# Performance work log

Measured on AMD Instinct MI355X. Metric: run time of the kernel, lower is better.

The kernel has to match this reference:

```python
import jax, jax.numpy as jnp
import numpy as np

DECAY = 0.99
EPS = 1e-05
COMMIT_COST = 0.25


def setup_inputs() -> dict:
    key = jax.random.key(0)
    k1, k2 = jax.random.split(key)
    z = jax.random.normal(k1, (32, 256, 64, 64), dtype=jnp.float32)
    codebook = jax.random.normal(k2, (512, 256), dtype=jnp.float32)
    n_i = jnp.zeros((512,), dtype=jnp.float32)
    e_i = codebook  # register_buffer('e_i', codebook.data.clone())
    return {"z": z, "codebook": codebook, "n_i": n_i, "e_i": e_i}


def reference(z, codebook, n_i, e_i):
    K, D = codebook.shape
    b = z.shape[0]
    flat = z.reshape(-1, D)  # [N, D]

    dist = (
        jnp.sum(flat * flat, axis=1, keepdims=True)
        + jnp.sum(codebook * codebook, axis=1)
        - 2.0 * (flat @ codebook.T)
    )  # [N, K]
    encoding = jnp.argmin(dist, axis=1)  # [N]

    # one-hot matmul gather == direct gather
    code = codebook[encoding].reshape(z.shape)

    # EMA codebook update (training path, no-grad in the original)
    counts = jax.ops.segment_sum(
        jnp.ones((flat.shape[0],), dtype=flat.dtype), encoding, num_segments=K
    )  # idx.sum(0)
    code_update = jax.ops.segment_sum(flat, encoding, num_segments=K)  # idx.T @ flat
    n_new = DECAY * n_i + (1.0 - DECAY) * counts
    n_new = (n_new + EPS) / (b + K * EPS) * b  # Laplace smoothing (uses batch size b)
    e_new = DECAY * e_i + (1.0 - DECAY) * code_update
    codebook_new = e_new / n_new[:, None]

    commitment_loss = COMMIT_COST * jnp.mean(
        (z - jax.lax.stop_gradient(code)) ** 2
    )
    # straight-through estimator
    code_ste = z + jax.lax.stop_gradient(code - z)
    return (code_ste, commitment_loss, encoding, codebook_new, n_new, e_new)
```

## Files before the change

### kernel.cpp

```cpp
#include <hip/hip_runtime.h>
#include <cfloat>

#define NROWS 131072
#define DIM 256
#define KCODES 512
#define DECAYF 0.99f
#define OMDECAYF 0.01f
#define EPSF 1e-5f
#define BATCHF 32.0f

#define CHUNK 128
#define ROWMASK 0x1FFFF

#define BMW 16
#define NWAVE 8
#define BMB (NWAVE * BMW)
#define PLANE_STRIDE (KCODES * DIM)
#define PLANE_BYTES (PLANE_STRIDE * 2)
#define PC2 16
#define NPIECE (KCODES / PC2)
#define PIECE_H_BYTES 8192
#define SBUF_HALF 16384

typedef __attribute__((ext_vector_type(8))) _Float16 half8;
typedef __attribute__((ext_vector_type(4))) float f32x4;


__device__ __forceinline__ void gload_lds16(const void* g, void* l) {
  __builtin_amdgcn_global_load_lds(
      (const __attribute__((address_space(1))) unsigned int*)g,
      (__attribute__((address_space(3))) unsigned int*)l, 16, 0, 0);
}

__global__ __launch_bounds__(256) void cnorm_kernel(const float* __restrict__ cb,
                                                    const float* __restrict__ e_i,
                                                    float* __restrict__ cnorm,
                                                    float* __restrict__ en_out,
                                                    unsigned short* __restrict__ planes,
                                                    int* __restrict__ counts,
                                                    int* __restrict__ off,
                                                    float* __restrict__ loss_acc) {
  int k = blockIdx.x;
  int t = threadIdx.x;
  if (t == 0) {
    counts[k] = 0;
    off[k] = 0;
    if (k == 0) loss_acc[0] = 0.f;
  }
  size_t idx = (size_t)k * DIM + t;
  float v = cb[idx];
  en_out[idx] = DECAYF * e_i[idx];
  _Float16 h = (_Float16)v;
  float r1 = v - (float)h;
  _Float16 m = (_Float16)r1;
  unsigned short hb, mb;
  __builtin_memcpy(&hb, &h, 2);
  __builtin_memcpy(&mb, &m, 2);
  int tile = k >> 4, cl = k & 15;
  int kc = t >> 5, lk = (t >> 3) & 3, j = t & 7;
  size_t faddr = ((size_t)((tile * 8 + kc) * 64 + lk * 16 + cl)) * 8 + j;
  planes[faddr] = hb;
  planes[PLANE_STRIDE + faddr] = mb;
  float s = v * v;
  for (int o = 32; o > 0; o >>= 1) s += __shfl_down(s, o);
  __shared__ float p[4];
  if ((t & 63) == 0) p[t >> 6] = s;
  __syncthreads();
  if (t == 0) cnorm[k] = (p[0] + p[1]) + (p[2] + p[3]);
}

__global__ __launch_bounds__(512, 4) void argmin_kernel(
    const float* __restrict__ z, const unsigned short* __restrict__ planes,
    const float* __restrict__ cnorm, const float* __restrict__ cb,
    int* __restrict__ enc_int, float* __restrict__ enc_out,
    int* __restrict__ counts, float* __restrict__ code_out,
    float* __restrict__ loss_acc) {
  __shared__ __align__(16) unsigned char sbuf[2 * SBUF_HALF];
  __shared__ float cn_s[KCODES];
  __shared__ int hist[KCODES];
  __shared__ int sm_enc[BMB];
  __shared__ float lds_loss;

  const int tid = threadIdx.x;
  const int w = tid >> 6;
  const int l = tid & 63;
  const int lc = l & 15;
  const int lk = l >> 4;

  hist[tid] = 0;
  cn_s[tid] = cnorm[tid];
  if (tid == 0) lds_loss = 0.f;

  half8 a_h[8], a_m[8];
  float zn = 0.f;
  {
    int row = blockIdx.x * BMB + w * BMW + lc;
    const float* zr = z + (size_t)row * DIM;
#pragma unroll
    for (int ch = 0; ch < 8; ++ch) {
      float4 v0 = *(const float4*)&zr[ch * 32 + lk * 8];
      float4 v1 = *(const float4*)&zr[ch * 32 + lk * 8 + 4];
      float vv[8] = {v0.x, v0.y, v0.z, v0.w, v1.x, v1.y, v1.z, v1.w};
      half8 hh, mm;
#pragma unroll
      for (int j = 0; j < 8; ++j) {
        float f = vv[j];
        zn += f * f;
        _Float16 hb = (_Float16)f;
        float r1 = f - (float)hb;
        hh[j] = hb;
        mm[j] = (_Float16)r1;
      }
      a_h[ch] = hh; a_m[ch] = mm;
    }
  }
  zn += __shfl_xor(zn, 16);
  zn += __shfl_xor(zn, 32);

  float minv[4];
  int mini[4];
#pragma unroll
  for (int q = 0; q < 4; ++q) { minv[q] = FLT_MAX; mini[q] = 0; }

  const unsigned char* gplanes = (const unsigned char*)planes;

#define STAGE(p, b)                                                              \
  {                                                                              \
    const unsigned char* gh = gplanes + (size_t)(p) * PIECE_H_BYTES;             \
    unsigned char* lb = &sbuf[(b) * SBUF_HALF];                                  \
    _Pragma("unroll")                                                            \
    for (int q = 0; q < 2; ++q) {                                                \
      int c = w * 2 + q;                                                         \
      const unsigned char* g = (w < 4)                                           \
          ? gh + c * 1024 + l * 16                                               \
          : gh + PLANE_BYTES + (c - 8) * 1024 + l * 16;                          \
      gload_lds16(g, lb + c * 1024);                                             \
    }                                                                            \
  }

  STAGE(0, 0);
  __syncthreads();

#pragma unroll 1
  for (int p = 0; p < NPIECE; ++p) {
    const int cur = p & 1;
    if (p + 1 < NPIECE) STAGE(p + 1, cur ^ 1);

    const int lbase = cur * SBUF_HALF;
    f32x4 acc_a = {0.f, 0.f, 0.f, 0.f};
    f32x4 acc_b = {0.f, 0.f, 0.f, 0.f};
#pragma unroll
    for (int kc = 0; kc < 8; ++kc) {
      int o = lbase + kc * 1024 + l * 16;
      half8 bh = *(const half8*)&sbuf[o];
      half8 bm = *(const half8*)&sbuf[o + 8192];
      acc_a = __builtin_amdgcn_mfma_f32_16x16x32_f16(a_h[kc], bh, acc_a, 0, 0, 0);
      acc_b = __builtin_amdgcn_mfma_f32_16x16x32_f16(a_m[kc], bh, acc_b, 0, 0, 0);
      acc_a = __builtin_amdgcn_mfma_f32_16x16x32_f16(a_h[kc], bm, acc_a, 0, 0, 0);
    }
    {
      int code = p * PC2 + lc;
      float cn = cn_s[code];
#pragma unroll
      for (int q = 0; q < 4; ++q) {
        float s0 = cn - 2.f * (acc_a[q] + acc_b[q]);
        if (s0 < minv[q]) { minv[q] = s0; mini[q] = code; }
      }
    }
    __syncthreads();
  }
#undef STAGE


  float lsum = 0.f;
#pragma unroll
  for (int q = 0; q < 4; ++q) {
    float v = minv[q];
    int idx = mini[q];
    for (int o = 1; o < 16; o <<= 1) {
      float ov = __shfl_xor(v, o);
      int oi = __shfl_xor(idx, o);
      if (ov < v || (ov == v && oi < idx)) { v = ov; idx = oi; }
    }
    float znq = __shfl(zn, lk * 4 + q);
    if (lc == 0) {
      int rloc = w * BMW + lk * 4 + q;
      int row = blockIdx.x * BMB + rloc;
      enc_int[row] = idx;
      enc_out[row] = (float)idx;
      sm_enc[rloc] = idx;
      atomicAdd(&hist[idx], 1);
      lsum += znq + v;
    }
  }
  {
    float val = (lc == 0) ? lsum : 0.f;
    val += __shfl_xor(val, 16);
    val += __shfl_xor(val, 32);
    if (l == 0) atomicAdd(&lds_loss, val);
  }
  __syncthreads();

  {
    const float4* cb4 = (const float4*)cb;
    float4* out4 = (float4*)code_out;
    int base = blockIdx.x * (BMB * (DIM / 4));
#pragma unroll
    for (int it = 0; it < 16; ++it) {
      int idx = it * 512 + tid;
      int k = sm_enc[idx >> 6];
      out4[base + idx] = cb4[k * (DIM / 4) + (idx & 63)];
    }
  }

  {
    int h0 = hist[tid];
    if (h0) atomicAdd(&counts[tid], h0);
  }
  if (tid == 0) atomicAdd(loss_acc, lds_loss);
}

__global__ __launch_bounds__(256) void scatter_kernel(
    const int* __restrict__ enc, const int* __restrict__ counts,
    int* __restrict__ off, int* __restrict__ rowlist) {
  __shared__ int lcnt[KCODES];
  __shared__ int lbase[KCODES];
  __shared__ int pref[KCODES];
  int tid = threadIdx.x;
  int row = blockIdx.x * 256 + tid;
  lcnt[tid] = 0;
  lcnt[tid + 256] = 0;
  pref[tid] = counts[tid];
  pref[tid + 256] = counts[tid + 256];
  __syncthreads();
  int k = enc[row];
  int p = atomicAdd(&lcnt[k], 1);
  for (int o = 1; o < KCODES; o <<= 1) {
    int v0 = (tid >= o) ? pref[tid - o] : 0;
    int v1 = (tid + 256 >= o) ? pref[tid + 256 - o] : 0;
    __syncthreads();
    pref[tid] += v0;
    pref[tid + 256] += v1;
    __syncthreads();
  }
  int c0 = lcnt[tid];
  if (c0) lbase[tid] = (pref[tid] - counts[tid]) + atomicAdd(&off[tid], c0);
  int c1 = lcnt[tid + 256];
  if (c1) lbase[tid + 256] = (pref[tid + 256] - counts[tid + 256]) + atomicAdd(&off[tid + 256], c1);
  __syncthreads();
  rowlist[lbase[k] + p] = (k << 17) | row;
}

__global__ __launch_bounds__(256) void chunk_sum_kernel(
    const float* __restrict__ z, const int* __restrict__ rowlist,
    float* __restrict__ en_out) {
  __shared__ int rl[CHUNK];
  int tid = threadIdx.x;
  int d = tid;
  if (tid < CHUNK) rl[tid] = rowlist[blockIdx.x * CHUNK + tid];
  __syncthreads();
  int cur = rl[0] >> 17;
  float s = 0.f;
  for (int i = 0; i < CHUNK; i += 4) {
    int p0 = rl[i + 0], p1 = rl[i + 1], p2 = rl[i + 2], p3 = rl[i + 3];
    float v0 = z[(size_t)(p0 & ROWMASK) * DIM + d];
    float v1 = z[(size_t)(p1 & ROWMASK) * DIM + d];
    float v2 = z[(size_t)(p2 & ROWMASK) * DIM + d];
    float v3 = z[(size_t)(p3 & ROWMASK) * DIM + d];
    int k;
    k = p0 >> 17;
    if (k != cur) { atomicAdd(&en_out[(size_t)cur * DIM + d], OMDECAYF * s); s = 0.f; cur = k; }
    s += v0;
    k = p1 >> 17;
    if (k != cur) { atomicAdd(&en_out[(size_t)cur * DIM + d], OMDECAYF * s); s = 0.f; cur = k; }
    s += v1;
    k = p2 >> 17;
    if (k != cur) { atomicAdd(&en_out[(size_t)cur * DIM + d], OMDECAYF * s); s = 0.f; cur = k; }
    s += v2;
    k = p3 >> 17;
    if (k != cur) { atomicAdd(&en_out[(size_t)cur * DIM + d], OMDECAYF * s); s = 0.f; cur = k; }
    s += v3;
  }
  atomicAdd(&en_out[(size_t)cur * DIM + d], OMDECAYF * s);
}

__global__ __launch_bounds__(256) void finalize_kernel(
    const float* __restrict__ en, const int* __restrict__ counts,
    const float* __restrict__ n_i, float* __restrict__ nn_out,
    float* __restrict__ cbn_out, const float* __restrict__ loss_acc,
    float* __restrict__ loss_out) {
  int k = blockIdx.x;
  int d = threadIdx.x;
  float nn = DECAYF * n_i[k] + OMDECAYF * (float)counts[k];
  nn = (nn + EPSF) / (BATCHF + (float)KCODES * EPSF) * BATCHF;
  if (d == 0) nn_out[k] = nn;
  size_t idx = (size_t)k * DIM + d;
  cbn_out[idx] = en[idx] / nn;
  if (k == 0 && d == 0) loss_out[0] = 0.25f * loss_acc[0] / 33554432.0f;
}

extern "C" void kernel_launch(void* const* d_in, const int* in_sizes, int n_in,
                              void* d_out, int out_size, void* d_ws, size_t ws_size,
                              hipStream_t stream) {
  const float* z = (const float*)d_in[0];
  const float* cb = (const float*)d_in[1];
  const float* n_i = (const float*)d_in[2];
  const float* e_i = (const float*)d_in[3];

  float* out = (float*)d_out;
  float* out_code = out;
  float* out_loss = out + 33554432;
  float* out_enc = out + 33554433;
  float* out_cbn = out + 33685505;
  float* out_nn = out + 33816577;
  float* out_en = out + 33817089;

  char* ws = (char*)d_ws;
  float* cnorm = (float*)(ws + 0);
  int* counts = (int*)(ws + 2048);
  float* loss_acc = (float*)(ws + 4096);
  int* off = (int*)(ws + 6144);
  int* enc_int = (int*)(ws + 12288);
  int* rowlist = (int*)(ws + 536576);
  unsigned short* planes = (unsigned short*)(ws + 536576);

  cnorm_kernel<<<KCODES, 256, 0, stream>>>(cb, e_i, cnorm, out_en, planes,
                                           counts, off, loss_acc);
  argmin_kernel<<<NROWS / BMB, 512, 0, stream>>>(z, planes, cnorm, cb, enc_int,
                                                 out_enc, counts, out_code, loss_acc);
  scatter_kernel<<<NROWS / 256, 256, 0, stream>>>(enc_int, counts, off, rowlist);
  chunk_sum_kernel<<<NROWS / CHUNK, 256, 0, stream>>>(z, rowlist, out_en);
  finalize_kernel<<<KCODES, 256, 0, stream>>>(out_en, counts, n_i, out_nn,
                                              out_cbn, loss_acc, out_loss);
}
```

Before: 362.5 us.

## Triple-buffer codebook pieces with explicit vmcnt waits and MFMA priority

```diff
diff --git a/kernel.cpp b/kernel.cpp
--- a/kernel.cpp
+++ b/kernel.cpp
@@ -21,6 +21,7 @@
 #define NPIECE (KCODES / PC2)
 #define PIECE_H_BYTES 8192
 #define SBUF_HALF 16384
+#define NBUF 3
 
 typedef __attribute__((ext_vector_type(8))) _Float16 half8;
 typedef __attribute__((ext_vector_type(4))) float f32x4;
@@ -75,11 +76,9 @@
     int* __restrict__ enc_int, float* __restrict__ enc_out,
     int* __restrict__ counts, float* __restrict__ code_out,
     float* __restrict__ loss_acc) {
-  __shared__ __align__(16) unsigned char sbuf[2 * SBUF_HALF];
+  __shared__ __align__(16) unsigned char sbuf[NBUF * SBUF_HALF];
   __shared__ float cn_s[KCODES];
-  __shared__ int hist[KCODES];
   __shared__ int sm_enc[BMB];
-  __shared__ float lds_loss;
 
   const int tid = threadIdx.x;
   const int w = tid >> 6;
@@ -87,9 +86,7 @@
   const int lc = l & 15;
   const int lk = l >> 4;
 
-  hist[tid] = 0;
   cn_s[tid] = cnorm[tid];
-  if (tid == 0) lds_loss = 0.f;
 
   half8 a_h[8], a_m[8];
   float zn = 0.f;
@@ -138,38 +135,51 @@
     }                                                                            \
   }
 
+#define COMPUTE(p)                                                               \
+  {                                                                              \
+    const int lbase = ((p) % NBUF) * SBUF_HALF;                                  \
+    f32x4 acc_a = {0.f, 0.f, 0.f, 0.f};                                          \
+    f32x4 acc_b = {0.f, 0.f, 0.f, 0.f};                                          \
+    __builtin_amdgcn_s_setprio(1);                                               \
+    _Pragma("unroll")                                                            \
+    for (int kc = 0; kc < 8; ++kc) {                                             \
+      int o = lbase + kc * 1024 + l * 16;                                        \
+      half8 bh = *(const half8*)&sbuf[o];                                        \
+      half8 bm = *(const half8*)&sbuf[o + 8192];                                 \
+      acc_a = __builtin_amdgcn_mfma_f32_16x16x32_f16(a_h[kc], bh, acc_a, 0, 0, 0); \
+      acc_b = __builtin_amdgcn_mfma_f32_16x16x32_f16(a_m[kc], bh, acc_b, 0, 0, 0); \
+      acc_a = __builtin_amdgcn_mfma_f32_16x16x32_f16(a_h[kc], bm, acc_a, 0, 0, 0); \
+    }                                                                            \
+    __builtin_amdgcn_s_setprio(0);                                               \
+    int code = (p) * PC2 + lc;                                                   \
+    float cn = cn_s[code];                                                       \
+    _Pragma("unroll")                                                            \
+    for (int q = 0; q < 4; ++q) {                                                \
+      float s0 = cn - 2.f * (acc_a[q] + acc_b[q]);                               \
+      if (s0 < minv[q]) { minv[q] = s0; mini[q] = code; }                        \
+    }                                                                            \
+  }
+
   STAGE(0, 0);
+  STAGE(1, 1);
   __syncthreads();
 
 #pragma unroll 1
-  for (int p = 0; p < NPIECE; ++p) {
-    const int cur = p & 1;
-    if (p + 1 < NPIECE) STAGE(p + 1, cur ^ 1);
-
-    const int lbase = cur * SBUF_HALF;
-    f32x4 acc_a = {0.f, 0.f, 0.f, 0.f};
-    f32x4 acc_b = {0.f, 0.f, 0.f, 0.f};
-#pragma unroll
-    for (int kc = 0; kc < 8; ++kc) {
-      int o = lbase + kc * 1024 + l * 16;
-      half8 bh = *(const half8*)&sbuf[o];
-      half8 bm = *(const half8*)&sbuf[o + 8192];
-      acc_a = __builtin_amdgcn_mfma_f32_16x16x32_f16(a_h[kc], bh, acc_a, 0, 0, 0);
-      acc_b = __builtin_amdgcn_mfma_f32_16x16x32_f16(a_m[kc], bh, acc_b, 0, 0, 0);
-      acc_a = __builtin_amdgcn_mfma_f32_16x16x32_f16(a_h[kc], bm, acc_a, 0, 0, 0);
-    }
-    {
-      int code = p * PC2 + lc;
-      float cn = cn_s[code];
-#pragma unroll
-      for (int q = 0; q < 4; ++q) {
-        float s0 = cn - 2.f * (acc_a[q] + acc_b[q]);
-        if (s0 < minv[q]) { minv[q] = s0; mini[q] = code; }
-      }
-    }
-    __syncthreads();
-  }
+  for (int p = 0; p < NPIECE - 1; ++p) {
+    if (p) {
+      asm volatile("s_waitcnt vmcnt(2)" ::: "memory");
+      __builtin_amdgcn_s_barrier();
+      __builtin_amdgcn_sched_barrier(0);
+    }
+    if (p + 2 < NPIECE) STAGE(p + 2, (p + 2) % NBUF);
+    COMPUTE(p);
+  }
+  asm volatile("s_waitcnt vmcnt(0)" ::: "memory");
+  __builtin_amdgcn_s_barrier();
+  __builtin_amdgcn_sched_barrier(0);
+  COMPUTE(NPIECE - 1);
 #undef STAGE
+#undef COMPUTE
 
 
   float lsum = 0.f;
@@ -189,7 +199,7 @@
       enc_int[row] = idx;
       enc_out[row] = (float)idx;
       sm_enc[rloc] = idx;
-      atomicAdd(&hist[idx], 1);
+      atomicAdd(&counts[idx], 1);
       lsum += znq + v;
     }
   }
@@ -197,7 +207,7 @@
     float val = (lc == 0) ? lsum : 0.f;
     val += __shfl_xor(val, 16);
     val += __shfl_xor(val, 32);
-    if (l == 0) atomicAdd(&lds_loss, val);
+    if (l == 0) atomicAdd(loss_acc, val);
   }
   __syncthreads();
 
@@ -212,12 +222,6 @@
       out4[base + idx] = cb4[k * (DIM / 4) + (idx & 63)];
     }
   }
-
-  {
-    int h0 = hist[tid];
-    if (h0) atomicAdd(&counts[tid], h0);
-  }
-  if (tid == 0) atomicAdd(loss_acc, lds_loss);
 }
 
 __global__ __launch_bounds__(256) void scatter_kernel(
```

New measurement: 436.6 us. 20.4% more time.
